# Optimization experiments

Measured on AMD Instinct MI355X. Metric: run time of the kernel, lower is better.

## Reference

```python
import jax, jax.numpy as jnp
import numpy as np

# Mesh sizes: level-7 icosphere input, level-6 mesh for this Down block
VIN = 163842   # input vertices (level 7)
V = 40962      # nv_prev: vertices of down mesh (level 6)
F = 2 * V - 4  # 81920 faces
B, CIN, COUT = 4, 32, 64
DEG_L, DEG_G, DEG_F = 7, 3, 6  # nnz per row of L, G, F2V
EPS = 1e-5


def spmm(x, rows, cols, vals, nrows):
    """Sparse (nrows x K) @ dense x[B,C,K] -> [B,C,nrows] via gather + segment_sum."""
    g = x[..., cols] * vals                      # [B, C, nnz]
    b, c, nnz = g.shape
    out = jax.ops.segment_sum(g.reshape(b * c, nnz).T, rows,
                              num_segments=nrows, indices_are_sorted=True)
    return out.T.reshape(b, c, nrows)


def mesh_conv(x, coeffs, bias, Lrow, Lcol, Lval, Grow, Gcol, Gval,
              Frow, Fcol, Fval, EW, NS):
    # x: [B, C, V]
    identity = x
    lap = spmm(x, Lrow, Lcol, Lval, V)                       # [B,C,V]
    gf = spmm(x, Grow, Gcol, Gval, 3 * F)                    # [B,C,3F]
    b, c = x.shape[:2]
    gf = gf.reshape(b, c, 3, F).transpose(0, 1, 3, 2)        # [B,C,F,3]
    grad_ew = jnp.sum(gf * EW, axis=-1)                      # [B,C,F]
    grad_ns = jnp.sum(gf * NS, axis=-1)                      # [B,C,F]
    gv_ew = spmm(grad_ew, Frow, Fcol, Fval, V)               # [B,C,V]
    gv_ns = spmm(grad_ns, Frow, Fcol, Fval, V)               # [B,C,V]
    feat = jnp.stack([identity, lap, gv_ew, gv_ns], axis=-1)  # [B,C,V,4]
    return jnp.einsum('oik,bivk->bov', coeffs, feat) + bias[None, :, None]


def bn_relu(x, gamma, beta):
    # BatchNorm1d training mode: stats over (batch, vertex), biased variance
    mu = jnp.mean(x, axis=(0, 2), keepdims=True)
    var = jnp.var(x, axis=(0, 2), keepdims=True)
    xn = (x - mu) * jax.lax.rsqrt(var + EPS)
    return jax.nn.relu(xn * gamma[None, :, None] + beta[None, :, None])


def setup_inputs() -> dict:
    key = jax.random.key(0)
    ks = jax.random.split(key, 16)
    x = jax.random.normal(ks[0], (B, CIN, VIN), dtype=jnp.float32)
    # Sparse Laplacian L: V x V, 7 nnz per row (self + 6 neighbors)
    Lrow = jnp.repeat(jnp.arange(V, dtype=jnp.int32), DEG_L)
    Lcol = jax.random.randint(ks[1], (V * DEG_L,), 0, V, dtype=jnp.int32)
    Lval = jax.random.normal(ks[2], (V * DEG_L,), dtype=jnp.float32) * 0.1
    # Sparse gradient G: 3F x V, 3 nnz per row (face's 3 vertices)
    Grow = jnp.repeat(jnp.arange(3 * F, dtype=jnp.int32), DEG_G)
    Gcol = jax.random.randint(ks[3], (3 * F * DEG_G,), 0, V, dtype=jnp.int32)
    Gval = jax.random.normal(ks[4], (3 * F * DEG_G,), dtype=jnp.float32) * 0.1
    # Sparse face->vertex averaging F2V: V x F, 6 nnz per row
    Frow = jnp.repeat(jnp.arange(V, dtype=jnp.int32), DEG_F)
    Fcol = jax.random.randint(ks[5], (V * DEG_F,), 0, F, dtype=jnp.int32)
    Fval = jnp.full((V * DEG_F,), 1.0 / DEG_F, dtype=jnp.float32)
    # Face tangent basis vectors
    EW = jax.random.normal(ks[6], (F, 3), dtype=jnp.float32)
    NS = jax.random.normal(ks[7], (F, 3), dtype=jnp.float32)
    # Learned params: two MeshConv + two BatchNorm1d
    coeffs1 = jax.random.normal(ks[8], (COUT, CIN, 4), dtype=jnp.float32) * 0.1
    bias1 = jnp.zeros((COUT,), dtype=jnp.float32)
    gamma1 = jnp.ones((COUT,), dtype=jnp.float32)
    beta1 = jnp.zeros((COUT,), dtype=jnp.float32)
    coeffs2 = jax.random.normal(ks[9], (COUT, COUT, 4), dtype=jnp.float32) * 0.1
    bias2 = jnp.zeros((COUT,), dtype=jnp.float32)
    gamma2 = jnp.ones((COUT,), dtype=jnp.float32)
    beta2 = jnp.zeros((COUT,), dtype=jnp.float32)
    return dict(x=x, Lrow=Lrow, Lcol=Lcol, Lval=Lval, Grow=Grow, Gcol=Gcol,
                Gval=Gval, Frow=Frow, Fcol=Fcol, Fval=Fval, EW=EW, NS=NS,
                coeffs1=coeffs1, bias1=bias1, gamma1=gamma1, beta1=beta1,
                coeffs2=coeffs2, bias2=bias2, gamma2=gamma2, beta2=beta2)


def reference(x, Lrow, Lcol, Lval, Grow, Gcol, Gval, Frow, Fcol, Fval, EW, NS,
              coeffs1, bias1, gamma1, beta1, coeffs2, bias2, gamma2, beta2):
    # Down: restrict to coarser mesh vertices, then DoubleConv
    h = x[:, :, :V]
    h = mesh_conv(h, coeffs1, bias1, Lrow, Lcol, Lval, Grow, Gcol, Gval,
                  Frow, Fcol, Fval, EW, NS)
    h = bn_relu(h, gamma1, beta1)
    h = mesh_conv(h, coeffs2, bias2, Lrow, Lcol, Lval, Grow, Gcol, Gval,
                  Frow, Fcol, Fval, EW, NS)
    h = bn_relu(h, gamma2, beta2)
    return h
```

## Files before the change

### kernel.cpp

```cpp
#include <hip/hip_runtime.h>
#include <hip/hip_bf16.h>
#include <stdint.h>

#define NV    40962
#define NVIN  163842
#define NB    4
#define NCIN  32
#define NCOUT 64
#define NF    81920

typedef __attribute__((ext_vector_type(8))) short short8;
typedef __attribute__((ext_vector_type(4))) float f32x4;

static __device__ __forceinline__ uint32_t f2bf_rne(float f) {
  uint32_t u = __float_as_uint(f);
  return (u + 0x7fffu + ((u >> 16) & 1u)) >> 16;
}
static __device__ __forceinline__ float bf_lo(uint32_t u) { return __uint_as_float(u << 16); }
static __device__ __forceinline__ float bf_hi(uint32_t u) { return __uint_as_float(u & 0xffff0000u); }

__global__ __launch_bounds__(256) void k_transpose(const float* __restrict__ x,
                                                   uint32_t* __restrict__ xt32) {
  const int nvt = (NV + 63) >> 6;
  int bb = blockIdx.x / nvt;
  int v0 = (blockIdx.x % nvt) << 6;
  __shared__ float t[NCIN][65];
  int vi = threadIdx.x & 63, cg = threadIdx.x >> 6;
  int v = v0 + vi;
  for (int c = cg; c < NCIN; c += 4)
    t[c][vi] = (v < NV) ? x[(size_t)(bb * NCIN + c) * NVIN + v] : 0.f;
  __syncthreads();
  for (int i = threadIdx.x; i < 64 * 16; i += 256) {
    int v2 = i >> 4, cp = i & 15;
    int vv = v0 + v2;
    if (vv < NV)
      xt32[(size_t)vv * 64 + bb * 16 + cp] =
          (f2bf_rne(t[2 * cp + 1][v2]) << 16) | f2bf_rne(t[2 * cp][v2]);
  }
}

template <int C>
__global__ __launch_bounds__(256) void k_grad(const uint32_t* __restrict__ xin32,
                                              const int* __restrict__ Gcol,
                                              const float* __restrict__ Gval,
                                              const float* __restrict__ EW,
                                              const float* __restrict__ NS,
                                              uint64_t* __restrict__ gg64) {
  constexpr int BC2 = NB * C / 2;
  constexpr int FP = 256 / BC2;
  const int p = threadIdx.x % BC2;
  const int fs = threadIdx.x / BC2;
  for (int f0 = blockIdx.x * FP; f0 < NF; f0 += gridDim.x * FP) {
    int f = f0 + fs;
    float e0 = 0, e1 = 0, n0 = 0, n1 = 0;
#pragma unroll
    for (int k = 0; k < 3; ++k) {
      int r = k * NF + f;
      float g0 = 0, g1 = 0;
#pragma unroll
      for (int e = 0; e < 3; ++e) {
        int colv = Gcol[r * 3 + e];
        float wv = Gval[r * 3 + e];
        uint32_t u = xin32[(size_t)colv * BC2 + p];
        g0 += wv * bf_lo(u);
        g1 += wv * bf_hi(u);
      }
      float ew = EW[f * 3 + k], ns = NS[f * 3 + k];
      e0 += g0 * ew; n0 += g0 * ns;
      e1 += g1 * ew; n1 += g1 * ns;
    }
    uint32_t a = (f2bf_rne(n0) << 16) | f2bf_rne(e0);
    uint32_t b = (f2bf_rne(n1) << 16) | f2bf_rne(e1);
    gg64[(size_t)f * BC2 + p] = ((uint64_t)b << 32) | a;
  }
}

template <int C>
__global__ __launch_bounds__(256) void k_conv_mfma(
    const uint32_t* __restrict__ xin32,
    const int* __restrict__ Lcol, const float* __restrict__ Lval,
    const int* __restrict__ Fcol, const float* __restrict__ Fval,
    const uint64_t* __restrict__ gg64,
    const float* __restrict__ coeffs,
    const float* __restrict__ bias,
    uint16_t* __restrict__ hout,
    float* __restrict__ bnS, float* __restrict__ bnQ) {
  constexpr int BC2 = NB * C / 2;
  constexpr int K = 4 * C;
  constexpr int K2 = 2 * K;
  constexpr int KS = K / 32;
  constexpr int VG = (C == 64) ? 8 : 16;
  constexpr int M = 4 * VG;
  constexpr int MT = M / 16;
  constexpr int WPM = 4 / MT;
  constexpr int NTC = MT;
  constexpr int VSTEP = 256 / BC2;

  __shared__ uint4 sA4[(M * K2) / 16];
  __shared__ uint4 sB4[4 * KS * 64];
  __shared__ float sS[64], sQ[64];

  for (int u = threadIdx.x; u < 4 * KS * 64; u += 256) {
    int lane = u & 63;
    int s = (u >> 6) % KS;
    int nt = (u >> 6) / KS;
    int o = nt * 16 + (lane & 15);
    int kb = s * 32 + (lane >> 4) * 8;
    const float* cp = coeffs + o * K + kb;
    uint4 wv;
    wv.x = (f2bf_rne(cp[1]) << 16) | f2bf_rne(cp[0]);
    wv.y = (f2bf_rne(cp[3]) << 16) | f2bf_rne(cp[2]);
    wv.z = (f2bf_rne(cp[5]) << 16) | f2bf_rne(cp[4]);
    wv.w = (f2bf_rne(cp[7]) << 16) | f2bf_rne(cp[6]);
    sB4[u] = wv;
  }
  if (threadIdx.x < 64) { sS[threadIdx.x] = 0.f; sQ[threadIdx.x] = 0.f; }

  const int tid = threadIdx.x;
  const int lane = tid & 63;
  const int w = tid >> 6;
  const int mtile = w / WPM;
  const int ntbase = (w % WPM) * NTC;
  const int col = lane & 15;
  const int lg = lane >> 4;

  const int p = tid % BC2;
  const int b = p / (C / 2);
  const int c0 = 2 * (p % (C / 2));
  const int vst = tid / BC2;

  float S[NTC], Q[NTC], bo[NTC];
#pragma unroll
  for (int t = 0; t < NTC; ++t) {
    S[t] = 0.f; Q[t] = 0.f;
    bo[t] = bias[(ntbase + t) * 16 + col];
  }
  __syncthreads();

  char* sA = (char*)sA4;
  const int npass = (NV + VG - 1) / VG;

  for (int it = blockIdx.x; it < npass; it += gridDim.x) {
    const int v0 = it * VG;
#pragma unroll
    for (int step = 0; step < VG / VSTEP; ++step) {
      int vl = step * VSTEP + vst;
      int v = v0 + vl;
      int m = vl * 4 + b;
      uint4 outv = {0u, 0u, 0u, 0u};
      if (v < NV) {
        uint32_t uid = xin32[(size_t)v * BC2 + p];
        float id0 = bf_lo(uid), id1 = bf_hi(uid);
        float l0 = 0.f, l1 = 0.f;
#pragma unroll
        for (int d = 0; d < 7; ++d) {
          int colv = Lcol[v * 7 + d];
          float wv = Lval[v * 7 + d];
          uint32_t u = xin32[(size_t)colv * BC2 + p];
          l0 += wv * bf_lo(u);
          l1 += wv * bf_hi(u);
        }
        float e0 = 0, e1 = 0, n0 = 0, n1 = 0;
#pragma unroll
        for (int d = 0; d < 6; ++d) {
          int fc = Fcol[v * 6 + d];
          float fv = Fval[v * 6 + d];
          uint64_t g = gg64[(size_t)fc * BC2 + p];
          uint32_t ga = (uint32_t)g, gb = (uint32_t)(g >> 32);
          e0 += fv * bf_lo(ga); n0 += fv * bf_hi(ga);
          e1 += fv * bf_lo(gb); n1 += fv * bf_hi(gb);
        }
        outv.x = (f2bf_rne(l0) << 16) | f2bf_rne(id0);
        outv.y = (f2bf_rne(n0) << 16) | f2bf_rne(e0);
        outv.z = (f2bf_rne(l1) << 16) | f2bf_rne(id1);
        outv.w = (f2bf_rne(n1) << 16) | f2bf_rne(e1);
      }
      int byteoff = m * K2 + ((c0 * 8) ^ ((m & 7) << 4));
      *(uint4*)(sA + byteoff) = outv;
    }
    __syncthreads();

    f32x4 acc[NTC];
#pragma unroll
    for (int t = 0; t < NTC; ++t) acc[t] = (f32x4){0.f, 0.f, 0.f, 0.f};
    const int marow = mtile * 16 + col;
    const int abase = marow * K2;
    const int aswz = (marow & 7) << 4;
#pragma unroll
    for (int s = 0; s < KS; ++s) {
      int kb = s * 32 + lg * 8;
      short8 af = *(const short8*)(sA + abase + ((kb * 2) ^ aswz));
#pragma unroll
      for (int t = 0; t < NTC; ++t) {
        short8 bf = *(const short8*)&sB4[((ntbase + t) * KS + s) * 64 + lane];
        acc[t] = __builtin_amdgcn_mfma_f32_16x16x32_bf16(af, bf, acc[t], 0, 0, 0);
      }
    }

#pragma unroll
    for (int t = 0; t < NTC; ++t) {
      int o = (ntbase + t) * 16 + col;
#pragma unroll
      for (int r = 0; r < 4; ++r) {
        int m = mtile * 16 + lg * 4 + r;
        int vl = m >> 2, b2 = m & 3;
        int v = v0 + vl;
        if (v < NV) {
          float h = acc[t][r] + bo[t];
          hout[((size_t)v * 4 + b2) * 64 + o] = (uint16_t)f2bf_rne(h);
          S[t] += h;
          Q[t] += h * h;
        }
      }
    }
    __syncthreads();
  }

#pragma unroll
  for (int t = 0; t < NTC; ++t) {
    int o = (ntbase + t) * 16 + col;
    atomicAdd(&sS[o], S[t]);
    atomicAdd(&sQ[o], Q[t]);
  }
  __syncthreads();
  if (threadIdx.x < 64) {
    atomicAdd(&bnS[threadIdx.x], sS[threadIdx.x]);
    atomicAdd(&bnQ[threadIdx.x], sQ[threadIdx.x]);
  }
}

__global__ void k_bnfin(const float* __restrict__ S, const float* __restrict__ Q,
                        const float* __restrict__ gamma, const float* __restrict__ beta,
                        float* __restrict__ scale, float* __restrict__ shift) {
  int o = threadIdx.x;
  if (o < NCOUT) {
    const float n = (float)((size_t)NB * NV);
    float mu = S[o] / n;
    float var = Q[o] / n - mu * mu;
    float sc = gamma[o] * rsqrtf(var + 1e-5f);
    scale[o] = sc;
    shift[o] = beta[o] - mu * sc;
  }
}

__global__ __launch_bounds__(256) void k_apply(uint32_t* __restrict__ h,
                                               const float* __restrict__ scale,
                                               const float* __restrict__ shift) {
  const int N = NV * 32;
  for (int i = blockIdx.x * 256 + threadIdx.x; i < N; i += gridDim.x * 256) {
    uint4 u = ((uint4*)h)[i];
    int o0 = (i * 8) & 63;
    uint32_t* uu = &u.x;
#pragma unroll
    for (int j = 0; j < 4; ++j) {
      float lo = fmaxf(0.f, bf_lo(uu[j]) * scale[o0 + 2 * j] + shift[o0 + 2 * j]);
      float hi = fmaxf(0.f, bf_hi(uu[j]) * scale[o0 + 2 * j + 1] + shift[o0 + 2 * j + 1]);
      uu[j] = (f2bf_rne(hi) << 16) | f2bf_rne(lo);
    }
    ((uint4*)h)[i] = u;
  }
}

__global__ __launch_bounds__(256) void k_final(const uint16_t* __restrict__ h2,
                                               const float* __restrict__ scale,
                                               const float* __restrict__ shift,
                                               float* __restrict__ out) {
  const int nvt = (NV + 63) >> 6;
  int b = blockIdx.x / nvt;
  int v0 = (blockIdx.x % nvt) << 6;
  __shared__ float t[64][65];
  int o = threadIdx.x & 63, vg = threadIdx.x >> 6;
  float sc = scale[o], sh = shift[o];
  for (int vi = vg; vi < 64; vi += 4) {
    int v = v0 + vi;
    float val = 0.f;
    if (v < NV) {
      uint32_t u = h2[(size_t)v * (NB * NCOUT) + b * NCOUT + o];
      val = __uint_as_float(u << 16);
    }
    t[o][vi] = fmaxf(0.f, val * sc + sh);
  }
  __syncthreads();
  int vi2 = threadIdx.x & 63, og = threadIdx.x >> 6;
  int v = v0 + vi2;
  for (int o2 = og; o2 < 64; o2 += 4) {
    if (v < NV) out[((size_t)b * NCOUT + o2) * NV + v] = t[o2][vi2];
  }
}

extern "C" void kernel_launch(void* const* d_in, const int* in_sizes, int n_in,
                              void* d_out, int out_size, void* d_ws, size_t ws_size,
                              hipStream_t stream) {
  const float* x       = (const float*)d_in[0];
  const int*   Lcol    = (const int*)d_in[2];
  const float* Lval    = (const float*)d_in[3];
  const int*   Gcol    = (const int*)d_in[5];
  const float* Gval    = (const float*)d_in[6];
  const int*   Fcol    = (const int*)d_in[8];
  const float* Fval    = (const float*)d_in[9];
  const float* EW      = (const float*)d_in[10];
  const float* NS      = (const float*)d_in[11];
  const float* coeffs1 = (const float*)d_in[12];
  const float* bias1   = (const float*)d_in[13];
  const float* gamma1  = (const float*)d_in[14];
  const float* beta1   = (const float*)d_in[15];
  const float* coeffs2 = (const float*)d_in[16];
  const float* bias2   = (const float*)d_in[17];
  const float* gamma2  = (const float*)d_in[18];
  const float* beta2   = (const float*)d_in[19];
  float* out           = (float*)d_out;

  uint32_t* xt = (uint32_t*)d_ws;
  uint64_t* gg = (uint64_t*)(xt + (size_t)NV * 64);
  uint32_t* h1 = (uint32_t*)(gg + (size_t)NF * 128);
  uint32_t* h2 = h1 + (size_t)NV * 128;
  float*    st = (float*)(h2 + (size_t)NV * 128);
  float *S1 = st, *Q1 = st + 64, *S2 = st + 128, *Q2 = st + 192;
  float *sc1 = st + 256, *sh1 = st + 320, *sc2 = st + 384, *sh2 = st + 448;

  hipMemsetAsync(st, 0, 256 * sizeof(float), stream);

  const int nvt = (NV + 63) >> 6;
  k_transpose<<<NB * nvt, 256, 0, stream>>>(x, xt);

  k_grad<NCIN><<<2048, 256, 0, stream>>>(xt, Gcol, Gval, EW, NS, gg);
  k_conv_mfma<NCIN><<<2048, 256, 0, stream>>>(xt, Lcol, Lval, Fcol, Fval, gg,
                                              coeffs1, bias1, (uint16_t*)h1, S1, Q1);
  k_bnfin<<<1, 64, 0, stream>>>(S1, Q1, gamma1, beta1, sc1, sh1);
  k_apply<<<2048, 256, 0, stream>>>(h1, sc1, sh1);

  k_grad<NCOUT><<<2048, 256, 0, stream>>>(h1, Gcol, Gval, EW, NS, gg);
  k_conv_mfma<NCOUT><<<2048, 256, 0, stream>>>(h1, Lcol, Lval, Fcol, Fval, gg,
                                               coeffs2, bias2, (uint16_t*)h2, S2, Q2);
  k_bnfin<<<1, 64, 0, stream>>>(S2, Q2, gamma2, beta2, sc2, sh2);
  k_final<<<NB * nvt, 256, 0, stream>>>((const uint16_t*)h2, sc2, sh2, out);
}
```

Measured before the change: 496.2 us.

## Prepack MFMA weights once, batch sparse gathers, and scalarize row indices

```diff
diff --git a/kernel.cpp b/kernel.cpp
--- a/kernel.cpp
+++ b/kernel.cpp
@@ -39,6 +39,36 @@
   }
 }
 
+__global__ __launch_bounds__(256) void k_packB(const float* __restrict__ c1,
+                                               const float* __restrict__ c2,
+                                               uint4* __restrict__ pb1,
+                                               uint4* __restrict__ pb2) {
+  for (int u = threadIdx.x; u < 1024; u += 256) {
+    int lane = u & 63, s = (u >> 6) % 4, nt = (u >> 6) / 4;
+    int o = nt * 16 + (lane & 15);
+    int kb = s * 32 + (lane >> 4) * 8;
+    const float* cp = c1 + o * 128 + kb;
+    uint4 wv;
+    wv.x = (f2bf_rne(cp[1]) << 16) | f2bf_rne(cp[0]);
+    wv.y = (f2bf_rne(cp[3]) << 16) | f2bf_rne(cp[2]);
+    wv.z = (f2bf_rne(cp[5]) << 16) | f2bf_rne(cp[4]);
+    wv.w = (f2bf_rne(cp[7]) << 16) | f2bf_rne(cp[6]);
+    pb1[u] = wv;
+  }
+  for (int u = threadIdx.x; u < 2048; u += 256) {
+    int lane = u & 63, s = (u >> 6) % 8, nt = (u >> 6) / 8;
+    int o = nt * 16 + (lane & 15);
+    int kb = s * 32 + (lane >> 4) * 8;
+    const float* cp = c2 + o * 256 + kb;
+    uint4 wv;
+    wv.x = (f2bf_rne(cp[1]) << 16) | f2bf_rne(cp[0]);
+    wv.y = (f2bf_rne(cp[3]) << 16) | f2bf_rne(cp[2]);
+    wv.z = (f2bf_rne(cp[5]) << 16) | f2bf_rne(cp[4]);
+    wv.w = (f2bf_rne(cp[7]) << 16) | f2bf_rne(cp[6]);
+    pb2[u] = wv;
+  }
+}
+
 template <int C>
 __global__ __launch_bounds__(256) void k_grad(const uint32_t* __restrict__ xin32,
                                               const int* __restrict__ Gcol,
@@ -51,23 +81,32 @@
   const int p = threadIdx.x % BC2;
   const int fs = threadIdx.x / BC2;
   for (int f0 = blockIdx.x * FP; f0 < NF; f0 += gridDim.x * FP) {
-    int f = f0 + fs;
-    float e0 = 0, e1 = 0, n0 = 0, n1 = 0;
+    int f = __builtin_amdgcn_readfirstlane(f0 + fs);
+    int gc[9]; float gv[9];
 #pragma unroll
     for (int k = 0; k < 3; ++k) {
       int r = k * NF + f;
-      float g0 = 0, g1 = 0;
 #pragma unroll
       for (int e = 0; e < 3; ++e) {
-        int colv = Gcol[r * 3 + e];
-        float wv = Gval[r * 3 + e];
-        uint32_t u = xin32[(size_t)colv * BC2 + p];
-        g0 += wv * bf_lo(u);
-        g1 += wv * bf_hi(u);
+        gc[k * 3 + e] = Gcol[r * 3 + e];
+        gv[k * 3 + e] = Gval[r * 3 + e];
       }
-      float ew = EW[f * 3 + k], ns = NS[f * 3 + k];
-      e0 += g0 * ew; n0 += g0 * ns;
-      e1 += g1 * ew; n1 += g1 * ns;
+    }
+    uint32_t xs[9];
+#pragma unroll
+    for (int i = 0; i < 9; ++i) xs[i] = xin32[(size_t)gc[i] * BC2 + p];
+    float ew[3], ns[3];
+#pragma unroll
+    for (int k = 0; k < 3; ++k) { ew[k] = EW[f * 3 + k]; ns[k] = NS[f * 3 + k]; }
+    float e0 = 0, e1 = 0, n0 = 0, n1 = 0;
+#pragma unroll
+    for (int k = 0; k < 3; ++k) {
+      float g0 = gv[k * 3] * bf_lo(xs[k * 3]) + gv[k * 3 + 1] * bf_lo(xs[k * 3 + 1]) +
+                 gv[k * 3 + 2] * bf_lo(xs[k * 3 + 2]);
+      float g1 = gv[k * 3] * bf_hi(xs[k * 3]) + gv[k * 3 + 1] * bf_hi(xs[k * 3 + 1]) +
+                 gv[k * 3 + 2] * bf_hi(xs[k * 3 + 2]);
+      e0 += g0 * ew[k]; n0 += g0 * ns[k];
+      e1 += g1 * ew[k]; n1 += g1 * ns[k];
     }
     uint32_t a = (f2bf_rne(n0) << 16) | f2bf_rne(e0);
     uint32_t b = (f2bf_rne(n1) << 16) | f2bf_rne(e1);
@@ -76,12 +115,12 @@
 }
 
 template <int C>
-__global__ __launch_bounds__(256) void k_conv_mfma(
+__global__ __launch_bounds__(256, 6) void k_conv_mfma(
     const uint32_t* __restrict__ xin32,
     const int* __restrict__ Lcol, const float* __restrict__ Lval,
     const int* __restrict__ Fcol, const float* __restrict__ Fval,
     const uint64_t* __restrict__ gg64,
-    const float* __restrict__ coeffs,
+    const uint4* __restrict__ pB,
     const float* __restrict__ bias,
     uint16_t* __restrict__ hout,
     float* __restrict__ bnS, float* __restrict__ bnQ) {
@@ -97,23 +136,7 @@
   constexpr int VSTEP = 256 / BC2;
 
   __shared__ uint4 sA4[(M * K2) / 16];
-  __shared__ uint4 sB4[4 * KS * 64];
   __shared__ float sS[64], sQ[64];
-
-  for (int u = threadIdx.x; u < 4 * KS * 64; u += 256) {
-    int lane = u & 63;
-    int s = (u >> 6) % KS;
-    int nt = (u >> 6) / KS;
-    int o = nt * 16 + (lane & 15);
-    int kb = s * 32 + (lane >> 4) * 8;
-    const float* cp = coeffs + o * K + kb;
-    uint4 wv;
-    wv.x = (f2bf_rne(cp[1]) << 16) | f2bf_rne(cp[0]);
-    wv.y = (f2bf_rne(cp[3]) << 16) | f2bf_rne(cp[2]);
-    wv.z = (f2bf_rne(cp[5]) << 16) | f2bf_rne(cp[4]);
-    wv.w = (f2bf_rne(cp[7]) << 16) | f2bf_rne(cp[6]);
-    sB4[u] = wv;
-  }
   if (threadIdx.x < 64) { sS[threadIdx.x] = 0.f; sQ[threadIdx.x] = 0.f; }
 
   const int tid = threadIdx.x;
@@ -149,30 +172,34 @@
       int m = vl * 4 + b;
       uint4 outv = {0u, 0u, 0u, 0u};
       if (v < NV) {
-        uint32_t uid = xin32[(size_t)v * BC2 + p];
-        float id0 = bf_lo(uid), id1 = bf_hi(uid);
+        int vu = __builtin_amdgcn_readfirstlane(v);
+        uint32_t uid = xin32[(size_t)vu * BC2 + p];
+        int lc[7]; float lw[7];
+#pragma unroll
+        for (int d = 0; d < 7; ++d) { lc[d] = Lcol[vu * 7 + d]; lw[d] = Lval[vu * 7 + d]; }
+        uint32_t lx[7];
+#pragma unroll
+        for (int d = 0; d < 7; ++d) lx[d] = xin32[(size_t)lc[d] * BC2 + p];
+        int fc[6]; float fw[6];
+#pragma unroll
+        for (int d = 0; d < 6; ++d) { fc[d] = Fcol[vu * 6 + d]; fw[d] = Fval[vu * 6 + d]; }
+        uint64_t gx[6];
+#pragma unroll
+        for (int d = 0; d < 6; ++d) gx[d] = gg64[(size_t)fc[d] * BC2 + p];
+
         float l0 = 0.f, l1 = 0.f;
 #pragma unroll
-        for (int d = 0; d < 7; ++d) {
-          int colv = Lcol[v * 7 + d];
-          float wv = Lval[v * 7 + d];
-          uint32_t u = xin32[(size_t)colv * BC2 + p];
-          l0 += wv * bf_lo(u);
-          l1 += wv * bf_hi(u);
+        for (int d = 0; d < 7; ++d) { l0 += lw[d] * bf_lo(lx[d]); l1 += lw[d] * bf_hi(lx[d]); }
+        float e0 = 0, e1 = 0, n0 = 0, n1 = 0;
+#pragma unroll
+        for (int d = 0; d < 6; ++d) {
+          uint32_t ga = (uint32_t)gx[d], gb = (uint32_t)(gx[d] >> 32);
+          e0 += fw[d] * bf_lo(ga); n0 += fw[d] * bf_hi(ga);
+          e1 += fw[d] * bf_lo(gb); n1 += fw[d] * bf_hi(gb);
         }
-        float e0 = 0, e1 = 0, n0 = 0, n1 = 0;
-#pragma unroll
-        for (int d = 0; d < 6; ++d) {
-          int fc = Fcol[v * 6 + d];
-          float fv = Fval[v * 6 + d];
-          uint64_t g = gg64[(size_t)fc * BC2 + p];
-          uint32_t ga = (uint32_t)g, gb = (uint32_t)(g >> 32);
-          e0 += fv * bf_lo(ga); n0 += fv * bf_hi(ga);
-          e1 += fv * bf_lo(gb); n1 += fv * bf_hi(gb);
-        }
-        outv.x = (f2bf_rne(l0) << 16) | f2bf_rne(id0);
+        outv.x = (f2bf_rne(l0) << 16) | (uid & 0xffffu);
         outv.y = (f2bf_rne(n0) << 16) | f2bf_rne(e0);
-        outv.z = (f2bf_rne(l1) << 16) | f2bf_rne(id1);
+        outv.z = (f2bf_rne(l1) << 16) | (uid >> 16);
         outv.w = (f2bf_rne(n1) << 16) | f2bf_rne(e1);
       }
       int byteoff = m * K2 + ((c0 * 8) ^ ((m & 7) << 4));
@@ -192,7 +219,7 @@
       short8 af = *(const short8*)(sA + abase + ((kb * 2) ^ aswz));
 #pragma unroll
       for (int t = 0; t < NTC; ++t) {
-        short8 bf = *(const short8*)&sB4[((ntbase + t) * KS + s) * 64 + lane];
+        short8 bf = *(const short8*)(pB + ((ntbase + t) * KS + s) * 64 + lane);
         acc[t] = __builtin_amdgcn_mfma_f32_16x16x32_bf16(af, bf, acc[t], 0, 0, 0);
       }
     }
@@ -315,23 +342,26 @@
   uint32_t* h1 = (uint32_t*)(gg + (size_t)NF * 128);
   uint32_t* h2 = h1 + (size_t)NV * 128;
   float*    st = (float*)(h2 + (size_t)NV * 128);
+  uint4*    pb1 = (uint4*)(st + 512);
+  uint4*    pb2 = pb1 + 1024;
   float *S1 = st, *Q1 = st + 64, *S2 = st + 128, *Q2 = st + 192;
   float *sc1 = st + 256, *sh1 = st + 320, *sc2 = st + 384, *sh2 = st + 448;
 
   hipMemsetAsync(st, 0, 256 * sizeof(float), stream);
 
   const int nvt = (NV + 63) >> 6;
+  k_packB<<<1, 256, 0, stream>>>(coeffs1, coeffs2, pb1, pb2);
   k_transpose<<<NB * nvt, 256, 0, stream>>>(x, xt);
 
   k_grad<NCIN><<<2048, 256, 0, stream>>>(xt, Gcol, Gval, EW, NS, gg);
   k_conv_mfma<NCIN><<<2048, 256, 0, stream>>>(xt, Lcol, Lval, Fcol, Fval, gg,
-                                              coeffs1, bias1, (uint16_t*)h1, S1, Q1);
+                                              pb1, bias1, (uint16_t*)h1, S1, Q1);
   k_bnfin<<<1, 64, 0, stream>>>(S1, Q1, gamma1, beta1, sc1, sh1);
   k_apply<<<2048, 256, 0, stream>>>(h1, sc1, sh1);
 
   k_grad<NCOUT><<<2048, 256, 0, stream>>>(h1, Gcol, Gval, EW, NS, gg);
   k_conv_mfma<NCOUT><<<2048, 256, 0, stream>>>(h1, Lcol, Lval, Fcol, Fval, gg,
-                                               coeffs2, bias2, (uint16_t*)h2, S2, Q2);
+                                               pb2, bias2, (uint16_t*)h2, S2, Q2);
   k_bnfin<<<1, 64, 0, stream>>>(S2, Q2, gamma2, beta2, sc2, sh2);
   k_final<<<NB * nvt, 256, 0, stream>>>((const uint16_t*)h2, sc2, sh2, out);
 }
```

Measured after the change: 592.3 us. +19.4%, slower.
